# Kernel optimization log

Hardware: AMD Instinct MI355X
Metric: run time of the kernel (lower is better)

## Reference

```python
import jax, jax.numpy as jnp
import numpy as np
import math

IN_FEATURES = 4096
OUT_FEATURES = 4096
TOKENS = 8192


def hadamard(x):
    """Orthonormal fast Walsh-Hadamard transform along last dim (power of two)."""
    n = x.shape[-1]
    orig_shape = x.shape
    y = x.reshape(-1, n)
    h = 1
    while h < n:  # log2(n) butterfly steps (static loop, n known at trace time)
        y = y.reshape(-1, n // (2 * h), 2 * h)
        left = y[..., :h]
        right = y[..., h:2 * h]
        y = jnp.concatenate([left + right, left - right], axis=-1)
        y = y.reshape(-1, n)
        h *= 2
    return (y / math.sqrt(n)).reshape(orig_shape)


def setup_inputs() -> dict:
    key = jax.random.key(0)
    k1, k2, k3, k4 = jax.random.split(key, 4)
    x = jax.random.normal(k1, (TOKENS, IN_FEATURES), dtype=jnp.float32)
    # int8-valued quantized weights, stored as int32 for portability
    Q_tilde = jax.random.randint(k2, (OUT_FEATURES, IN_FEATURES), -127, 128, dtype=jnp.int32)
    # per-row scales, positive, realistic magnitude (~max_abs/127)
    s_tilde = jax.random.uniform(k3, (OUT_FEATURES, 1), dtype=jnp.float32, minval=0.001, maxval=0.02)
    bias = jax.random.normal(k4, (OUT_FEATURES,), dtype=jnp.float32)
    return {"x": x, "Q_tilde": Q_tilde, "s_tilde": s_tilde, "bias": bias}


def reference(x, Q_tilde, s_tilde, bias):
    # y = hadamard(x) @ (Q * s)^T + bias
    xh = hadamard(x)                                      # [T, in]
    W = Q_tilde.astype(jnp.float32) * s_tilde             # [out, in] dequantized
    y = xh @ W.T + bias                                   # [T, out]
    return y
```

## Files before the change

### kernel.cpp

```cpp
#include <hip/hip_runtime.h>
#include <hip/hip_bf16.h>

typedef int   i32x4 __attribute__((ext_vector_type(4)));
typedef unsigned int   u32;
typedef unsigned short u16;
typedef signed char    i8;

#define TOKENS 8192
#define NDIM   4096
#define KDIM   4096
#define BK     64
#define NKT    (KDIM / BK)

__global__ __launch_bounds__(64)
void fwht_rows_q8(const float* __restrict__ x, i8* __restrict__ xq,
                  float* __restrict__ xscale) {
  const int row = blockIdx.x;
  const int l   = threadIdx.x;

  const float4* xv = reinterpret_cast<const float4*>(x + (size_t)row * KDIM) + l * 16;
  float v[64];
#pragma unroll
  for (int j = 0; j < 16; ++j) {
    float4 f = xv[j];
    v[4*j+0] = f.x; v[4*j+1] = f.y; v[4*j+2] = f.z; v[4*j+3] = f.w;
  }

#pragma unroll
  for (int h = 1; h < 64; h <<= 1) {
#pragma unroll
    for (int j = 0; j < 64; ++j) {
      if ((j & h) == 0) {
        float a = v[j], b = v[j + h];
        v[j] = a + b; v[j + h] = a - b;
      }
    }
  }

#pragma unroll
  for (int m = 1; m < 64; m <<= 1) {
    const bool up = (l & m) != 0;
#pragma unroll
    for (int j = 0; j < 64; ++j) {
      float p = __shfl_xor(v[j], m, 64);
      v[j] = up ? (p - v[j]) : (v[j] + p);
    }
  }

  float mxu = 0.f;
#pragma unroll
  for (int j = 0; j < 64; ++j) mxu = fmaxf(mxu, fabsf(v[j]));
#pragma unroll
  for (int m = 1; m < 64; m <<= 1) mxu = fmaxf(mxu, __shfl_xor(mxu, m, 64));
  mxu = fmaxf(mxu, 1e-30f);
  const float inv = 127.0f / mxu;

  i8* orow = xq + (size_t)row * KDIM + l * 64;
#pragma unroll
  for (int g = 0; g < 4; ++g) {
    u32 w[4];
#pragma unroll
    for (int q4 = 0; q4 < 4; ++q4) {
      int b0 = __float2int_rn(v[g*16+q4*4+0] * inv);
      int b1 = __float2int_rn(v[g*16+q4*4+1] * inv);
      int b2 = __float2int_rn(v[g*16+q4*4+2] * inv);
      int b3 = __float2int_rn(v[g*16+q4*4+3] * inv);
      b0 = min(127, max(-127, b0)); b1 = min(127, max(-127, b1));
      b2 = min(127, max(-127, b2)); b3 = min(127, max(-127, b3));
      w[q4] = (u32)(b0 & 0xff) | ((u32)(b1 & 0xff) << 8) |
              ((u32)(b2 & 0xff) << 16) | ((u32)(b3 & 0xff) << 24);
    }
    uint4 pk; pk.x = w[0]; pk.y = w[1]; pk.z = w[2]; pk.w = w[3];
    *reinterpret_cast<uint4*>(orow + g * 16) = pk;
  }
  if (l == 0) xscale[row] = mxu * (0.015625f / 127.0f);
}

__device__ __forceinline__ u32 pack4(int4 q) {
  return (u32)(q.x & 0xff) | ((u32)(q.y & 0xff) << 8) |
         ((u32)(q.z & 0xff) << 16) | ((u32)(q.w & 0xff) << 24);
}
__global__ __launch_bounds__(256)
void qpack(const int* __restrict__ Q, i8* __restrict__ W8) {
  const size_t idx = ((size_t)blockIdx.x * 256 + threadIdx.x) * 16;
  int4 a = *reinterpret_cast<const int4*>(Q + idx);
  int4 b = *reinterpret_cast<const int4*>(Q + idx + 4);
  int4 c = *reinterpret_cast<const int4*>(Q + idx + 8);
  int4 d = *reinterpret_cast<const int4*>(Q + idx + 12);
  uint4 pk; pk.x = pack4(a); pk.y = pack4(b); pk.z = pack4(c); pk.w = pack4(d);
  *reinterpret_cast<uint4*>(W8 + idx) = pk;
}

__global__ __launch_bounds__(512, 2)
void gemm256_i8(const i8* __restrict__ A, const i8* __restrict__ B,
                const float* __restrict__ xscale, const float* __restrict__ s,
                const float* __restrict__ bias, float* __restrict__ C) {
  __shared__ __align__(16) i8 lds[4 * 32768];

  const int th   = threadIdx.x;
  const int wave = th >> 6;
  const int lane = th & 63;

  const int b0 = blockIdx.x;
  const int xc = b0 & 7;
  const int i  = b0 >> 3;
  const int mt = i >> 1;
  const int nt = xc * 2 + (i & 1);

  const int srow = th >> 2;
  const int scol = ((th & 3) * 16) ^ (((th >> 5) & 1) << 5);
  const i8* gA0 = A + (size_t)(mt * 256 + srow) * KDIM + scol;
  const i8* gA1 = gA0 + (size_t)128 * KDIM;
  const i8* gB0 = B + (size_t)(nt * 256 + srow) * KDIM + scol;
  const i8* gB1 = gB0 + (size_t)128 * KDIM;

  const int ldsA0 = wave * 1024;
  const int ldsA1 = 8192 + wave * 1024;
  const int ldsB0 = 16384 + wave * 1024;
  const int ldsB1 = 24576 + wave * 1024;

#define STAGE_A(tt, ss) do {                                                    \
    __builtin_amdgcn_global_load_lds(                                           \
      (const __attribute__((address_space(1))) void*)(gA0 + (size_t)(tt) * BK), \
      (__attribute__((address_space(3))) void*)(lds + (ss) * 32768 + ldsA0), 16, 0, 0); \
    __builtin_amdgcn_global_load_lds(                                           \
      (const __attribute__((address_space(1))) void*)(gA1 + (size_t)(tt) * BK), \
      (__attribute__((address_space(3))) void*)(lds + (ss) * 32768 + ldsA1), 16, 0, 0); \
  } while (0)
#define STAGE_B(tt, ss) do {                                                    \
    __builtin_amdgcn_global_load_lds(                                           \
      (const __attribute__((address_space(1))) void*)(gB0 + (size_t)(tt) * BK), \
      (__attribute__((address_space(3))) void*)(lds + (ss) * 32768 + ldsB0), 16, 0, 0); \
    __builtin_amdgcn_global_load_lds(                                           \
      (const __attribute__((address_space(1))) void*)(gB1 + (size_t)(tt) * BK), \
      (__attribute__((address_space(3))) void*)(lds + (ss) * 32768 + ldsB1), 16, 0, 0); \
  } while (0)

  const int wm = wave >> 2;
  const int wn = wave & 3;
  const int laneRow = lane & 15;
  const int kByte   = (lane >> 4) << 4;
  const int swz     = ((lane >> 3) & 1) << 5;
  const int aOff = (((wm * 128 + laneRow) * 64 + kByte) ^ swz);
  const int bOff = (((wn * 64 + laneRow) * 64 + kByte) ^ swz) + 16384;

  i32x4 acc[8][4];
#pragma unroll
  for (int mi = 0; mi < 8; ++mi)
#pragma unroll
    for (int ni = 0; ni < 4; ++ni)
      acc[mi][ni] = i32x4{0, 0, 0, 0};

  STAGE_A(0, 0); STAGE_B(0, 0);
  STAGE_A(1, 1); STAGE_B(1, 1);
  asm volatile("s_waitcnt vmcnt(4)" ::: "memory");
  __builtin_amdgcn_sched_barrier(0);
  __builtin_amdgcn_s_barrier();

  i32x4 afA[4], afB[4], bf0[4], bf1[4];
  {
    const char* c0 = (const char*)lds;
#pragma unroll
    for (int ni = 0; ni < 4; ++ni)
      bf0[ni] = *(const i32x4*)(c0 + bOff + ni * 1024);
#pragma unroll
    for (int mi = 0; mi < 4; ++mi)
      afA[mi] = *(const i32x4*)(c0 + aOff + mi * 1024);
  }

#define TILE(t, BFC, BFN) do {                                                  \
    const char* cur = (const char*)lds + ((t) & 3) * 32768;                     \
    const char* nxt = (const char*)lds + (((t) + 1) & 3) * 32768;               \
                              \
    _Pragma("unroll")                                                           \
    for (int mi = 0; mi < 4; ++mi)                                              \
      afB[mi] = *(const i32x4*)(cur + aOff + 4096 + mi * 1024);                 \
    if ((t) + 2 < NKT) STAGE_A((t) + 2, ((t) + 2) & 3);                         \
    asm volatile("s_waitcnt lgkmcnt(4)" ::: "memory");       \
    __builtin_amdgcn_sched_barrier(0);                                          \
    __builtin_amdgcn_s_setprio(1);                                              \
    _Pragma("unroll")                                                           \
    for (int mi = 0; mi < 4; ++mi)                                              \
      _Pragma("unroll")                                                         \
      for (int ni = 0; ni < 4; ++ni)                                            \
        acc[mi][ni] = __builtin_amdgcn_mfma_i32_16x16x64_i8(afA[mi], BFC[ni],   \
                                                            acc[mi][ni], 0, 0, 0); \
    __builtin_amdgcn_s_setprio(0);                                              \
    if ((t) + 1 < NKT) {                                                        \
      if ((t) + 2 < NKT) { asm volatile("s_waitcnt vmcnt(2)" ::: "memory"); }   \
      else               { asm volatile("s_waitcnt vmcnt(0)" ::: "memory"); }   \
      __builtin_amdgcn_sched_barrier(0);                                        \
      __builtin_amdgcn_s_barrier();          \
      _Pragma("unroll")                                                         \
      for (int ni = 0; ni < 4; ++ni)                                            \
        BFN[ni] = *(const i32x4*)(nxt + bOff + ni * 1024);                      \
      _Pragma("unroll")                                                         \
      for (int mi = 0; mi < 4; ++mi)                                            \
        afA[mi] = *(const i32x4*)(nxt + aOff + mi * 1024);                      \
      if ((t) + 2 < NKT) STAGE_B((t) + 2, ((t) + 2) & 3);                       \
      asm volatile("s_waitcnt lgkmcnt(8)" ::: "memory");         \
      __builtin_amdgcn_sched_barrier(0);                                        \
    } else {                                                                    \
      asm volatile("s_waitcnt lgkmcnt(0)" ::: "memory");                        \
      __builtin_amdgcn_sched_barrier(0);                                        \
    }                                                                           \
    __builtin_amdgcn_s_setprio(1);                                              \
    _Pragma("unroll")                                                           \
    for (int mi = 0; mi < 4; ++mi)                                              \
      _Pragma("unroll")                                                         \
      for (int ni = 0; ni < 4; ++ni)                                            \
        acc[mi + 4][ni] = __builtin_amdgcn_mfma_i32_16x16x64_i8(afB[mi], BFC[ni], \
                                                            acc[mi + 4][ni], 0, 0, 0); \
    __builtin_amdgcn_s_setprio(0);                                              \
  } while (0)

  for (int t = 0; t < NKT; t += 2) {
    TILE(t,     bf0, bf1);
    TILE(t + 1, bf1, bf0);
  }
#undef TILE
#undef STAGE_A
#undef STAGE_B

  const int col0 = nt * 256 + wn * 64 + (lane & 15);
  const int row0 = mt * 256 + wm * 128 + ((lane >> 4) << 2);
  float xs[4][8];
#pragma unroll
  for (int mi = 0; mi < 8; ++mi)
#pragma unroll
    for (int r = 0; r < 4; ++r)
      xs[r][mi] = xscale[row0 + mi * 16 + r];
#pragma unroll
  for (int ni = 0; ni < 4; ++ni) {
    const float sc = s[col0 + ni * 16];
    const float bv = bias[col0 + ni * 16];
#pragma unroll
    for (int mi = 0; mi < 8; ++mi) {
      float* cp = C + (size_t)(row0 + mi * 16) * NDIM + col0 + ni * 16;
#pragma unroll
      for (int r = 0; r < 4; ++r)
        cp[(size_t)r * NDIM] = (float)acc[mi][ni][r] * (xs[r][mi] * sc) + bv;
    }
  }
}

extern "C" void kernel_launch(void* const* d_in, const int* in_sizes, int n_in,
                              void* d_out, int out_size, void* d_ws, size_t ws_size,
                              hipStream_t stream) {
  (void)in_sizes; (void)n_in; (void)out_size; (void)ws_size;
  const float* x    = (const float*)d_in[0];
  const int*   Q    = (const int*)d_in[1];
  const float* s    = (const float*)d_in[2];
  const float* bias = (const float*)d_in[3];
  float* out = (float*)d_out;

  i8*    xq     = (i8*)d_ws;
  i8*    W8     = xq + (size_t)TOKENS * KDIM;
  float* xscale = (float*)(W8 + (size_t)NDIM * KDIM);

  fwht_rows_q8<<<dim3(TOKENS), dim3(64), 0, stream>>>(x, xq, xscale);
  qpack<<<dim3((NDIM * KDIM) / (256 * 16)), dim3(256), 0, stream>>>(Q, W8);
  gemm256_i8<<<dim3((TOKENS / 256) * (NDIM / 256)), dim3(512), 0, stream>>>(
      xq, W8, xscale, s, bias, out);
}
```

Baseline: 204.7 us.

## Fuse FWHT and weight-pack kernels; deepen GEMM prefetch to three tiles ahead

Merges the per-row Hadamard/quantize kernel and the int32-to-int8 weight pack into one launch, with 4 rows per 256-thread block and extra blocks doing the packing. This removes one launch and lets the two memory-bound phases overlap. The GEMM now issues all A and B loads for tile t+3 together after one barrier, giving a 3-deep prefetch in the 4-slot LDS ring. This hides more global latency but changes the waitcnt accounting, and slot reuse safety now rests on the barrier placement.

```diff
diff --git a/kernel.cpp b/kernel.cpp
--- a/kernel.cpp
+++ b/kernel.cpp
@@ -11,12 +11,29 @@
 #define KDIM   4096
 #define BK     64
 #define NKT    (KDIM / BK)
-
-__global__ __launch_bounds__(64)
-void fwht_rows_q8(const float* __restrict__ x, i8* __restrict__ xq,
-                  float* __restrict__ xscale) {
-  const int row = blockIdx.x;
-  const int l   = threadIdx.x;
+#define SLOT   32768
+
+__device__ __forceinline__ u32 pack4(int4 q) {
+  return (u32)(q.x & 0xff) | ((u32)(q.y & 0xff) << 8) |
+         ((u32)(q.z & 0xff) << 16) | ((u32)(q.w & 0xff) << 24);
+}
+
+__global__ __launch_bounds__(256)
+void fused_aux(const float* __restrict__ x, i8* __restrict__ xq,
+               float* __restrict__ xscale,
+               const int* __restrict__ Q, i8* __restrict__ W8) {
+  if (blockIdx.x >= 2048) {
+    const size_t idx = (((size_t)(blockIdx.x - 2048)) * 256 + threadIdx.x) * 16;
+    int4 a = *reinterpret_cast<const int4*>(Q + idx);
+    int4 b = *reinterpret_cast<const int4*>(Q + idx + 4);
+    int4 c = *reinterpret_cast<const int4*>(Q + idx + 8);
+    int4 d = *reinterpret_cast<const int4*>(Q + idx + 12);
+    uint4 pk; pk.x = pack4(a); pk.y = pack4(b); pk.z = pack4(c); pk.w = pack4(d);
+    *reinterpret_cast<uint4*>(W8 + idx) = pk;
+    return;
+  }
+  const int row = blockIdx.x * 4 + (threadIdx.x >> 6);
+  const int l   = threadIdx.x & 63;
 
   const float4* xv = reinterpret_cast<const float4*>(x + (size_t)row * KDIM) + l * 16;
   float v[64];
@@ -76,26 +93,11 @@
   if (l == 0) xscale[row] = mxu * (0.015625f / 127.0f);
 }
 
-__device__ __forceinline__ u32 pack4(int4 q) {
-  return (u32)(q.x & 0xff) | ((u32)(q.y & 0xff) << 8) |
-         ((u32)(q.z & 0xff) << 16) | ((u32)(q.w & 0xff) << 24);
-}
-__global__ __launch_bounds__(256)
-void qpack(const int* __restrict__ Q, i8* __restrict__ W8) {
-  const size_t idx = ((size_t)blockIdx.x * 256 + threadIdx.x) * 16;
-  int4 a = *reinterpret_cast<const int4*>(Q + idx);
-  int4 b = *reinterpret_cast<const int4*>(Q + idx + 4);
-  int4 c = *reinterpret_cast<const int4*>(Q + idx + 8);
-  int4 d = *reinterpret_cast<const int4*>(Q + idx + 12);
-  uint4 pk; pk.x = pack4(a); pk.y = pack4(b); pk.z = pack4(c); pk.w = pack4(d);
-  *reinterpret_cast<uint4*>(W8 + idx) = pk;
-}
-
 __global__ __launch_bounds__(512, 2)
-void gemm256_i8(const i8* __restrict__ A, const i8* __restrict__ B,
+void gemm_i8_dp(const i8* __restrict__ A, const i8* __restrict__ B,
                 const float* __restrict__ xscale, const float* __restrict__ s,
                 const float* __restrict__ bias, float* __restrict__ C) {
-  __shared__ __align__(16) i8 lds[4 * 32768];
+  __shared__ __align__(16) i8 lds[4 * SLOT];
 
   const int th   = threadIdx.x;
   const int wave = th >> 6;
@@ -119,21 +121,19 @@
   const int ldsB0 = 16384 + wave * 1024;
   const int ldsB1 = 24576 + wave * 1024;
 
-#define STAGE_A(tt, ss) do {                                                    \
+#define STAGE(tt, ss) do {                                                      \
     __builtin_amdgcn_global_load_lds(                                           \
       (const __attribute__((address_space(1))) void*)(gA0 + (size_t)(tt) * BK), \
-      (__attribute__((address_space(3))) void*)(lds + (ss) * 32768 + ldsA0), 16, 0, 0); \
+      (__attribute__((address_space(3))) void*)(lds + (ss) * SLOT + ldsA0), 16, 0, 0); \
     __builtin_amdgcn_global_load_lds(                                           \
       (const __attribute__((address_space(1))) void*)(gA1 + (size_t)(tt) * BK), \
-      (__attribute__((address_space(3))) void*)(lds + (ss) * 32768 + ldsA1), 16, 0, 0); \
-  } while (0)
-#define STAGE_B(tt, ss) do {                                                    \
+      (__attribute__((address_space(3))) void*)(lds + (ss) * SLOT + ldsA1), 16, 0, 0); \
     __builtin_amdgcn_global_load_lds(                                           \
       (const __attribute__((address_space(1))) void*)(gB0 + (size_t)(tt) * BK), \
-      (__attribute__((address_space(3))) void*)(lds + (ss) * 32768 + ldsB0), 16, 0, 0); \
+      (__attribute__((address_space(3))) void*)(lds + (ss) * SLOT + ldsB0), 16, 0, 0); \
     __builtin_amdgcn_global_load_lds(                                           \
       (const __attribute__((address_space(1))) void*)(gB1 + (size_t)(tt) * BK), \
-      (__attribute__((address_space(3))) void*)(lds + (ss) * 32768 + ldsB1), 16, 0, 0); \
+      (__attribute__((address_space(3))) void*)(lds + (ss) * SLOT + ldsB1), 16, 0, 0); \
   } while (0)
 
   const int wm = wave >> 2;
@@ -151,9 +151,8 @@
     for (int ni = 0; ni < 4; ++ni)
       acc[mi][ni] = i32x4{0, 0, 0, 0};
 
-  STAGE_A(0, 0); STAGE_B(0, 0);
-  STAGE_A(1, 1); STAGE_B(1, 1);
-  asm volatile("s_waitcnt vmcnt(4)" ::: "memory");
+  STAGE(0, 0); STAGE(1, 1); STAGE(2, 2);
+  asm volatile("s_waitcnt vmcnt(8)" ::: "memory");
   __builtin_amdgcn_sched_barrier(0);
   __builtin_amdgcn_s_barrier();
 
@@ -169,13 +168,11 @@
   }
 
 #define TILE(t, BFC, BFN) do {                                                  \
-    const char* cur = (const char*)lds + ((t) & 3) * 32768;                     \
-    const char* nxt = (const char*)lds + (((t) + 1) & 3) * 32768;               \
-                              \
+    const char* cur = (const char*)lds + ((t) & 3) * SLOT;                      \
+    const char* nxt = (const char*)lds + (((t) + 1) & 3) * SLOT;                \
     _Pragma("unroll")                                                           \
     for (int mi = 0; mi < 4; ++mi)                                              \
       afB[mi] = *(const i32x4*)(cur + aOff + 4096 + mi * 1024);                 \
-    if ((t) + 2 < NKT) STAGE_A((t) + 2, ((t) + 2) & 3);                         \
     asm volatile("s_waitcnt lgkmcnt(4)" ::: "memory");       \
     __builtin_amdgcn_sched_barrier(0);                                          \
     __builtin_amdgcn_s_setprio(1);                                              \
@@ -186,31 +183,30 @@
         acc[mi][ni] = __builtin_amdgcn_mfma_i32_16x16x64_i8(afA[mi], BFC[ni],   \
                                                             acc[mi][ni], 0, 0, 0); \
     __builtin_amdgcn_s_setprio(0);                                              \
+    if ((t) + 2 < NKT)      { asm volatile("s_waitcnt vmcnt(4)" ::: "memory"); } \
+    else if ((t) + 1 < NKT) { asm volatile("s_waitcnt vmcnt(0)" ::: "memory"); } \
+    __builtin_amdgcn_sched_barrier(0);                                          \
+    __builtin_amdgcn_s_barrier();                                               \
+    if ((t) + 3 < NKT) STAGE((t) + 3, ((t) + 3) & 3);                           \
     if ((t) + 1 < NKT) {                                                        \
-      if ((t) + 2 < NKT) { asm volatile("s_waitcnt vmcnt(2)" ::: "memory"); }   \
-      else               { asm volatile("s_waitcnt vmcnt(0)" ::: "memory"); }   \
-      __builtin_amdgcn_sched_barrier(0);                                        \
-      __builtin_amdgcn_s_barrier();          \
       _Pragma("unroll")                                                         \
       for (int ni = 0; ni < 4; ++ni)                                            \
         BFN[ni] = *(const i32x4*)(nxt + bOff + ni * 1024);                      \
       _Pragma("unroll")                                                         \
       for (int mi = 0; mi < 4; ++mi)                                            \
         afA[mi] = *(const i32x4*)(nxt + aOff + mi * 1024);                      \
-      if ((t) + 2 < NKT) STAGE_B((t) + 2, ((t) + 2) & 3);                       \
       asm volatile("s_waitcnt lgkmcnt(8)" ::: "memory");         \
-      __builtin_amdgcn_sched_barrier(0);                                        \
     } else {                                                                    \
       asm volatile("s_waitcnt lgkmcnt(0)" ::: "memory");                        \
-      __builtin_amdgcn_sched_barrier(0);                                        \
     }                                                                           \
+    __builtin_amdgcn_sched_barrier(0);                                          \
     __builtin_amdgcn_s_setprio(1);                                              \
     _Pragma("unroll")                                                           \
     for (int mi = 0; mi < 4; ++mi)                                              \
       _Pragma("unroll")                                                         \
       for (int ni = 0; ni < 4; ++ni)                                            \
         acc[mi + 4][ni] = __builtin_amdgcn_mfma_i32_16x16x64_i8(afB[mi], BFC[ni], \
-                                                            acc[mi + 4][ni], 0, 0, 0); \
+                                                        acc[mi + 4][ni], 0, 0, 0); \
     __builtin_amdgcn_s_setprio(0);                                              \
   } while (0)
 
@@ -219,8 +215,7 @@
     TILE(t + 1, bf1, bf0);
   }
 #undef TILE
-#undef STAGE_A
-#undef STAGE_B
+#undef STAGE
 
   const int col0 = nt * 256 + wn * 64 + (lane & 15);
   const int row0 = mt * 256 + wm * 128 + ((lane >> 4) << 2);
@@ -258,8 +253,7 @@
   i8*    W8     = xq + (size_t)TOKENS * KDIM;
   float* xscale = (float*)(W8 + (size_t)NDIM * KDIM);
 
-  fwht_rows_q8<<<dim3(TOKENS), dim3(64), 0, stream>>>(x, xq, xscale);
-  qpack<<<dim3((NDIM * KDIM) / (256 * 16)), dim3(256), 0, stream>>>(Q, W8);
-  gemm256_i8<<<dim3((TOKENS / 256) * (NDIM / 256)), dim3(512), 0, stream>>>(
+  fused_aux<<<dim3(6144), dim3(256), 0, stream>>>(x, xq, xscale, Q, W8);
+  gemm_i8_dp<<<dim3((TOKENS / 256) * (NDIM / 256)), dim3(512), 0, stream>>>(
       xq, W8, xscale, s, bias, out);
 }
```

Result: faster. 196.6 us (-4.0%).

## Fuse FWHT and weight-pack kernels; use an LDS transpose for the cross-lane butterflies

Applied to the files above, without the earlier changes.

The activation Hadamard/quantize kernel and the int32-to-int8 weight packing kernel are merged into one launch. The extra blocks at the end of the grid do the packing. Inside the FWHT, the six cross-lane shuffle butterfly stages are replaced by a padded LDS transpose followed by in-register butterflies, which removes 384 shuffles per thread. In exchange, the kernel uses about 66 KB of LDS per block, which limits occupancy, and the quantized output is written as 64 strided byte stores instead of four 16-byte vector stores.

```diff
diff --git a/kernel.cpp b/kernel.cpp
--- a/kernel.cpp
+++ b/kernel.cpp
@@ -12,11 +12,32 @@
 #define BK     64
 #define NKT    (KDIM / BK)
 
-__global__ __launch_bounds__(64)
-void fwht_rows_q8(const float* __restrict__ x, i8* __restrict__ xq,
-                  float* __restrict__ xscale) {
-  const int row = blockIdx.x;
-  const int l   = threadIdx.x;
+__device__ __forceinline__ u32 pack4(int4 q) {
+  return (u32)(q.x & 0xff) | ((u32)(q.y & 0xff) << 8) |
+         ((u32)(q.z & 0xff) << 16) | ((u32)(q.w & 0xff) << 24);
+}
+
+__global__ __launch_bounds__(256)
+void fused_aux(const float* __restrict__ x, i8* __restrict__ xq,
+               float* __restrict__ xscale,
+               const int* __restrict__ Q, i8* __restrict__ W8) {
+  __shared__ float tbuf[4 * 65 * 64];
+
+  if (blockIdx.x >= 2048) {
+    const size_t idx = (((size_t)(blockIdx.x - 2048)) * 256 + threadIdx.x) * 16;
+    int4 a = *reinterpret_cast<const int4*>(Q + idx);
+    int4 b = *reinterpret_cast<const int4*>(Q + idx + 4);
+    int4 c = *reinterpret_cast<const int4*>(Q + idx + 8);
+    int4 d = *reinterpret_cast<const int4*>(Q + idx + 12);
+    uint4 pk; pk.x = pack4(a); pk.y = pack4(b); pk.z = pack4(c); pk.w = pack4(d);
+    *reinterpret_cast<uint4*>(W8 + idx) = pk;
+    return;
+  }
+
+  const int wv  = threadIdx.x >> 6;
+  const int l   = threadIdx.x & 63;
+  const int row = blockIdx.x * 4 + wv;
+  float* lb = tbuf + wv * (65 * 64);
 
   const float4* xv = reinterpret_cast<const float4*>(x + (size_t)row * KDIM) + l * 16;
   float v[64];
@@ -38,57 +59,42 @@
   }
 
 #pragma unroll
-  for (int m = 1; m < 64; m <<= 1) {
-    const bool up = (l & m) != 0;
+  for (int j = 0; j < 64; ++j)
+    lb[l * 65 + j] = v[j];
+  asm volatile("s_waitcnt lgkmcnt(0)" ::: "memory");
+  __builtin_amdgcn_sched_barrier(0);
+  float w[64];
+#pragma unroll
+  for (int j = 0; j < 64; ++j)
+    w[j] = lb[j * 65 + l];
+
+#pragma unroll
+  for (int h = 1; h < 64; h <<= 1) {
 #pragma unroll
     for (int j = 0; j < 64; ++j) {
-      float p = __shfl_xor(v[j], m, 64);
-      v[j] = up ? (p - v[j]) : (v[j] + p);
+      if ((j & h) == 0) {
+        float a = w[j], b = w[j + h];
+        w[j] = a + b; w[j + h] = a - b;
+      }
     }
   }
 
   float mxu = 0.f;
 #pragma unroll
-  for (int j = 0; j < 64; ++j) mxu = fmaxf(mxu, fabsf(v[j]));
+  for (int j = 0; j < 64; ++j) mxu = fmaxf(mxu, fabsf(w[j]));
 #pragma unroll
   for (int m = 1; m < 64; m <<= 1) mxu = fmaxf(mxu, __shfl_xor(mxu, m, 64));
   mxu = fmaxf(mxu, 1e-30f);
   const float inv = 127.0f / mxu;
 
-  i8* orow = xq + (size_t)row * KDIM + l * 64;
-#pragma unroll
-  for (int g = 0; g < 4; ++g) {
-    u32 w[4];
-#pragma unroll
-    for (int q4 = 0; q4 < 4; ++q4) {
-      int b0 = __float2int_rn(v[g*16+q4*4+0] * inv);
-      int b1 = __float2int_rn(v[g*16+q4*4+1] * inv);
-      int b2 = __float2int_rn(v[g*16+q4*4+2] * inv);
-      int b3 = __float2int_rn(v[g*16+q4*4+3] * inv);
-      b0 = min(127, max(-127, b0)); b1 = min(127, max(-127, b1));
-      b2 = min(127, max(-127, b2)); b3 = min(127, max(-127, b3));
-      w[q4] = (u32)(b0 & 0xff) | ((u32)(b1 & 0xff) << 8) |
-              ((u32)(b2 & 0xff) << 16) | ((u32)(b3 & 0xff) << 24);
-    }
-    uint4 pk; pk.x = w[0]; pk.y = w[1]; pk.z = w[2]; pk.w = w[3];
-    *reinterpret_cast<uint4*>(orow + g * 16) = pk;
+  i8* orow = xq + (size_t)row * KDIM + l;
+#pragma unroll
+  for (int j = 0; j < 64; ++j) {
+    int b = __float2int_rn(w[j] * inv);
+    b = min(127, max(-127, b));
+    orow[j * 64] = (i8)b;
   }
   if (l == 0) xscale[row] = mxu * (0.015625f / 127.0f);
-}
-
-__device__ __forceinline__ u32 pack4(int4 q) {
-  return (u32)(q.x & 0xff) | ((u32)(q.y & 0xff) << 8) |
-         ((u32)(q.z & 0xff) << 16) | ((u32)(q.w & 0xff) << 24);
-}
-__global__ __launch_bounds__(256)
-void qpack(const int* __restrict__ Q, i8* __restrict__ W8) {
-  const size_t idx = ((size_t)blockIdx.x * 256 + threadIdx.x) * 16;
-  int4 a = *reinterpret_cast<const int4*>(Q + idx);
-  int4 b = *reinterpret_cast<const int4*>(Q + idx + 4);
-  int4 c = *reinterpret_cast<const int4*>(Q + idx + 8);
-  int4 d = *reinterpret_cast<const int4*>(Q + idx + 12);
-  uint4 pk; pk.x = pack4(a); pk.y = pack4(b); pk.z = pack4(c); pk.w = pack4(d);
-  *reinterpret_cast<uint4*>(W8 + idx) = pk;
 }
 
 __global__ __launch_bounds__(512, 2)
@@ -171,12 +177,11 @@
 #define TILE(t, BFC, BFN) do {                                                  \
     const char* cur = (const char*)lds + ((t) & 3) * 32768;                     \
     const char* nxt = (const char*)lds + (((t) + 1) & 3) * 32768;               \
-                              \
     _Pragma("unroll")                                                           \
     for (int mi = 0; mi < 4; ++mi)                                              \
       afB[mi] = *(const i32x4*)(cur + aOff + 4096 + mi * 1024);                 \
     if ((t) + 2 < NKT) STAGE_A((t) + 2, ((t) + 2) & 3);                         \
-    asm volatile("s_waitcnt lgkmcnt(4)" ::: "memory");       \
+    asm volatile("s_waitcnt lgkmcnt(4)" ::: "memory");                          \
     __builtin_amdgcn_sched_barrier(0);                                          \
     __builtin_amdgcn_s_setprio(1);                                              \
     _Pragma("unroll")                                                           \
@@ -190,7 +195,7 @@
       if ((t) + 2 < NKT) { asm volatile("s_waitcnt vmcnt(2)" ::: "memory"); }   \
       else               { asm volatile("s_waitcnt vmcnt(0)" ::: "memory"); }   \
       __builtin_amdgcn_sched_barrier(0);                                        \
-      __builtin_amdgcn_s_barrier();          \
+      __builtin_amdgcn_s_barrier();                                             \
       _Pragma("unroll")                                                         \
       for (int ni = 0; ni < 4; ++ni)                                            \
         BFN[ni] = *(const i32x4*)(nxt + bOff + ni * 1024);                      \
@@ -198,7 +203,7 @@
       for (int mi = 0; mi < 4; ++mi)                                            \
         afA[mi] = *(const i32x4*)(nxt + aOff + mi * 1024);                      \
       if ((t) + 2 < NKT) STAGE_B((t) + 2, ((t) + 2) & 3);                       \
-      asm volatile("s_waitcnt lgkmcnt(8)" ::: "memory");         \
+      asm volatile("s_waitcnt lgkmcnt(8)" ::: "memory");                        \
       __builtin_amdgcn_sched_barrier(0);                                        \
     } else {                                                                    \
       asm volatile("s_waitcnt lgkmcnt(0)" ::: "memory");                        \
@@ -258,8 +263,7 @@
   i8*    W8     = xq + (size_t)TOKENS * KDIM;
   float* xscale = (float*)(W8 + (size_t)NDIM * KDIM);
 
-  fwht_rows_q8<<<dim3(TOKENS), dim3(64), 0, stream>>>(x, xq, xscale);
-  qpack<<<dim3((NDIM * KDIM) / (256 * 16)), dim3(256), 0, stream>>>(Q, W8);
+  fused_aux<<<dim3(6144), dim3(256), 0, stream>>>(x, xq, xscale, Q, W8);
   gemm256_i8<<<dim3((TOKENS / 256) * (NDIM / 256)), dim3(512), 0, stream>>>(
       xq, W8, xscale, s, bias, out);
 }
```

Result: faster. 193.7 us (-5.4%).
